# Kernel tuning notes

Hardware: AMD Instinct MI355X
Metric: run time of the kernel (lower is better)

The kernel has to match this reference:

```python
import jax, jax.numpy as jnp
import numpy as np

N_MESH, N_GRID, N_EDGE = 2562, 16384, 49152
D, EDGE_DIM, OUT_DIM = 512, 4, 128
LN_EPS = 1e-5


def _mlp_ln(x, w1, b1, w2, b2, g, beta):
    # Linear -> ReLU -> Linear -> LayerNorm (activate_final=False, use_layer_norm=True)
    h = jax.nn.relu(x @ w1 + b1)
    h = h @ w2 + b2
    mu = jnp.mean(h, axis=-1, keepdims=True)
    var = jnp.var(h, axis=-1, keepdims=True)
    return (h - mu) * jax.lax.rsqrt(var + LN_EPS) * g + beta


def setup_inputs() -> dict:
    key = jax.random.key(0)
    ks = iter(jax.random.split(key, 40))

    def W(i, o):
        return (jax.random.normal(next(ks), (i, o), jnp.float32) / np.float32(np.sqrt(i)))

    inp = {
        "input_mesh_nodes": jax.random.normal(next(ks), (N_MESH, D), jnp.float32),
        "input_grid_nodes": jax.random.normal(next(ks), (N_GRID, D), jnp.float32),
        "input_edge_attr": jax.random.normal(next(ks), (N_EDGE, EDGE_DIM), jnp.float32),
        "edge_index": jnp.stack([
            jax.random.randint(next(ks), (N_EDGE,), 0, N_MESH, jnp.int32),  # senders (mesh)
            jax.random.randint(next(ks), (N_EDGE,), 0, N_GRID, jnp.int32),  # receivers (grid)
        ], axis=0),
        # edges_mlp: EDGE_DIM -> D -> D, LN
        "emlp_w1": W(EDGE_DIM, D), "emlp_b1": jnp.zeros((D,), jnp.float32),
        "emlp_w2": W(D, D), "emlp_b2": jnp.zeros((D,), jnp.float32),
        "emlp_g": jnp.ones((D,), jnp.float32), "emlp_beta": jnp.zeros((D,), jnp.float32),
        # gnn message MLP: 3D -> D -> D, LN   (cat(x_i, x_j, edge_attr))
        "ge_w1": W(3 * D, D), "ge_b1": jnp.zeros((D,), jnp.float32),
        "ge_w2": W(D, D), "ge_b2": jnp.zeros((D,), jnp.float32),
        "ge_g": jnp.ones((D,), jnp.float32), "ge_beta": jnp.zeros((D,), jnp.float32),
        # gnn node MLP: 2D -> D -> D, LN   (cat(receiver_x, aggr))
        "gn_w1": W(2 * D, D), "gn_b1": jnp.zeros((D,), jnp.float32),
        "gn_w2": W(D, D), "gn_b2": jnp.zeros((D,), jnp.float32),
        "gn_g": jnp.ones((D,), jnp.float32), "gn_beta": jnp.zeros((D,), jnp.float32),
        # grid_mlp_final: D -> D -> OUT_DIM, LN
        "fin_w1": W(D, D), "fin_b1": jnp.zeros((D,), jnp.float32),
        "fin_w2": W(D, OUT_DIM), "fin_b2": jnp.zeros((OUT_DIM,), jnp.float32),
        "fin_g": jnp.ones((OUT_DIM,), jnp.float32), "fin_beta": jnp.zeros((OUT_DIM,), jnp.float32),
    }
    return inp


def reference(input_mesh_nodes, input_grid_nodes, input_edge_attr, edge_index,
              emlp_w1, emlp_b1, emlp_w2, emlp_b2, emlp_g, emlp_beta,
              ge_w1, ge_b1, ge_w2, ge_b2, ge_g, ge_beta,
              gn_w1, gn_b1, gn_w2, gn_b2, gn_g, gn_beta,
              fin_w1, fin_b1, fin_w2, fin_b2, fin_g, fin_beta):
    # edge embedding MLP
    edges_emb = _mlp_ln(input_edge_attr, emlp_w1, emlp_b1, emlp_w2, emlp_b2, emlp_g, emlp_beta)
    senders, receivers = edge_index[0], edge_index[1]
    x_i = input_grid_nodes[receivers]   # receiver (grid) features gathered per edge
    x_j = input_mesh_nodes[senders]     # sender (mesh) features gathered per edge
    # per-edge message MLP on cat(x_i, x_j, edge_attr)
    msg = _mlp_ln(jnp.concatenate([x_i, x_j, edges_emb], axis=-1),
                  ge_w1, ge_b1, ge_w2, ge_b2, ge_g, ge_beta)  # [E, D]
    # scatter-add messages to receiver grid nodes (aggr='add')
    aggr = jax.ops.segment_sum(msg, receivers, num_segments=N_GRID)  # [N_GRID, D]
    # node update MLP on cat(receiver_x, aggr)
    gnn_out = _mlp_ln(jnp.concatenate([input_grid_nodes, aggr], axis=-1),
                      gn_w1, gn_b1, gn_w2, gn_b2, gn_g, gn_beta)
    latent_grid_nodes = input_grid_nodes + gnn_out  # residual
    return _mlp_ln(latent_grid_nodes, fin_w1, fin_b1, fin_w2, fin_b2, fin_g, fin_beta)
```

## Files before the change

kernel.cpp:

```cpp
#include <hip/hip_runtime.h>
#include <hip/hip_bf16.h>
#include <stdint.h>

#define LN_EPS 1e-5f

typedef __hip_bfloat16 bf16;
typedef short short8 __attribute__((ext_vector_type(8)));
typedef float f32x4 __attribute__((ext_vector_type(4)));

static __device__ __forceinline__ float bf2f(short s) {
    unsigned int u = ((unsigned int)(unsigned short)s) << 16;
    return __uint_as_float(u);
}
static __device__ __forceinline__ short f2bf(float x) {
    __hip_bfloat16 h = __float2bfloat16(x);
    return *reinterpret_cast<short*>(&h);
}

static __device__ __forceinline__ void gload16(const void* g, void* l) {
    __builtin_amdgcn_global_load_lds((const __attribute__((address_space(1))) void*)g,
                                     (__attribute__((address_space(3))) void*)l, 16, 0, 0);
}

struct TDesc { const float* src; bf16* dst; int K; int N; int kOff; const float* scale; };
struct TDescs { TDesc d[9]; };

__global__ void transpose_all_kernel(TDescs descs) {
    TDesc t = descs.d[blockIdx.z];
    int kb = blockIdx.x * 32, nb = blockIdx.y * 32;
    if (kb >= t.K || nb >= t.N) return;
    __shared__ float tile[32][33];
    int tx = threadIdx.x & 31, ty = threadIdx.x >> 5;
    for (int i = ty; i < 32; i += 8) {
        int k = kb + i, n = nb + tx;
        float v = (k < t.K && n < t.N) ? t.src[(size_t)(t.kOff + k) * t.N + n] : 0.f;
        if (t.scale && k < t.K) v *= t.scale[k];
        tile[i][tx] = v;
    }
    __syncthreads();
    for (int i = ty; i < 32; i += 8) {
        int n = nb + i, k = kb + tx;
        if (n < t.N && k < t.K)
            t.dst[(size_t)n * t.K + k] = __float2bfloat16(tile[tx][i]);
    }
}

__global__ void uv_kernel(const float* __restrict__ W, const float* __restrict__ g,
                          const float* __restrict__ be, float* __restrict__ u,
                          float* __restrict__ v) {
    int n = blockIdx.x * 256 + threadIdx.x;
    if (n >= 512) return;
    float su = 0.f, sv = 0.f;
    for (int k = 0; k < 512; k++) {
        float w = W[(size_t)(1024 + k) * 512 + n];
        su += g[k] * w;
        sv += be[k] * w;
    }
    u[n] = su;
    v[n] = sv;
}

__global__ void cvt_bf16_kernel(const float* __restrict__ src, bf16* __restrict__ dst, int n) {
    int i = blockIdx.x * 256 + threadIdx.x;
    int idx = i * 4;
    if (idx >= n) return;
    float4 v = *(const float4*)(src + idx);
    dst[idx + 0] = __float2bfloat16(v.x);
    dst[idx + 1] = __float2bfloat16(v.y);
    dst[idx + 2] = __float2bfloat16(v.z);
    dst[idx + 3] = __float2bfloat16(v.w);
}

__global__ void edge_l1_kernel(const float* __restrict__ attr, const float* __restrict__ w1,
                               const float* __restrict__ b1, bf16* __restrict__ h1, int E) {
    int e = blockIdx.x * 4 + (threadIdx.x >> 6);
    if (e >= E) return;
    int lane = threadIdx.x & 63;
    int d0 = lane * 8;
    float4 a = *(const float4*)(attr + (size_t)e * 4);
    float av[4] = {a.x, a.y, a.z, a.w};
    float s[8];
    {
        float4 c0 = *(const float4*)(b1 + d0), c1 = *(const float4*)(b1 + d0 + 4);
        s[0]=c0.x; s[1]=c0.y; s[2]=c0.z; s[3]=c0.w; s[4]=c1.x; s[5]=c1.y; s[6]=c1.z; s[7]=c1.w;
    }
#pragma unroll
    for (int k = 0; k < 4; k++) {
        float4 w0 = *(const float4*)(w1 + k * 512 + d0);
        float4 w1v = *(const float4*)(w1 + k * 512 + d0 + 4);
        float wv[8] = {w0.x, w0.y, w0.z, w0.w, w1v.x, w1v.y, w1v.z, w1v.w};
#pragma unroll
        for (int j = 0; j < 8; j++) s[j] += av[k] * wv[j];
    }
    short8 o;
#pragma unroll
    for (int j = 0; j < 8; j++) o[j] = f2bf(fmaxf(s[j], 0.f));
    *(short8*)(h1 + (size_t)e * 512 + d0) = o;
}

template <int EPI>
__global__ __launch_bounds__(512, 1) void gemm8_kernel(
    const bf16* __restrict__ A, const bf16* __restrict__ BT,
    const float* __restrict__ bias, bf16* __restrict__ C, int M, int N, int K,
    const bf16* __restrict__ gridp, const bf16* __restrict__ meshp,
    const int* __restrict__ send, const int* __restrict__ recv,
    const float2* __restrict__ stats, const float* __restrict__ uvec,
    const float* __restrict__ vvec) {
    __shared__ short SMEM[2 * (256 + 128) * 64];
    const int t = threadIdx.x;
    const int lane = t & 63, w = t >> 6;
    const int wm = w >> 1, wn = w & 1;
    const int lr = lane & 15, lh = lane >> 4;

    int gx = gridDim.x;
    int nwg = gx * gridDim.y;
    int orig = blockIdx.y * gx + blockIdx.x;
    int q = nwg >> 3, r = nwg & 7;
    int xcd = orig & 7, loc = orig >> 3;
    int wg = (xcd < r ? xcd * (q + 1) : r * (q + 1) + (xcd - r) * q) + loc;
    int bx = wg % gx, by = wg / gx;
    const int row0 = by * 256;
    const int col0 = bx * 128;

    const int sr3 = lane >> 3;
    const int su = (lane & 7) ^ sr3;
    const int scol = su * 8;
    const bf16* gaP[4];
    const bf16* gbP[2];
#pragma unroll
    for (int c = 0; c < 4; c++) {
        int ra = row0 + c * 64 + w * 8 + sr3; if (ra >= M) ra = M - 1;
        gaP[c] = A + (size_t)ra * K + scol;
    }
#pragma unroll
    for (int c = 0; c < 2; c++) {
        int rb = col0 + c * 64 + w * 8 + sr3; if (rb >= N) rb = N - 1;
        gbP[c] = BT + (size_t)rb * K + scol;
    }

    auto STAGE_A = [&](int b, int k0) {
        short* la = SMEM + b * 24576;
#pragma unroll
        for (int c = 0; c < 4; c++)
            gload16(gaP[c] + k0, la + (c * 64 + w * 8) * 64);
    };
    auto STAGE_B = [&](int b, int k0) {
        short* lb = SMEM + b * 24576 + 16384;
#pragma unroll
        for (int c = 0; c < 2; c++)
            gload16(gbP[c] + k0, lb + (c * 64 + w * 8) * 64);
    };

    f32x4 acc[4][4];
#pragma unroll
    for (int i = 0; i < 4; i++)
#pragma unroll
        for (int j = 0; j < 4; j++) acc[i][j] = {0.f, 0.f, 0.f, 0.f};

    const int T = K >> 6;
    STAGE_A(0, 0);
    STAGE_B(0, 0);

    for (int tt = 0; tt < T; ++tt) {
        const int bc = tt & 1;
        const int kn = (tt + 1) << 6;
        if (tt + 1 < T) {
            STAGE_A(bc ^ 1, kn);
            asm volatile("s_waitcnt vmcnt(4)" ::: "memory");
        } else {
            asm volatile("s_waitcnt vmcnt(0)" ::: "memory");
        }
        __builtin_amdgcn_s_barrier();

        const short* Ac = SMEM + bc * 24576;
        const short* Bc = Ac + 16384;

        {
            short8 af[4], bfv[4];
#pragma unroll
            for (int mf = 0; mf < 4; mf++) {
                int rowa = wm * 64 + mf * 16 + lr;
                int ua = lh ^ (rowa & 7);
                af[mf] = *(const short8*)&Ac[rowa * 64 + ua * 8];
            }
#pragma unroll
            for (int nf = 0; nf < 4; nf++) {
                int rowb = wn * 64 + nf * 16 + lr;
                int ub = lh ^ (rowb & 7);
                bfv[nf] = *(const short8*)&Bc[rowb * 64 + ub * 8];
            }
            asm volatile("" ::: "memory");
            __builtin_amdgcn_s_barrier();
            __builtin_amdgcn_s_setprio(1);
#pragma unroll
            for (int mf = 0; mf < 4; mf++)
#pragma unroll
                for (int nf = 0; nf < 4; nf++)
                    acc[mf][nf] = __builtin_amdgcn_mfma_f32_16x16x32_bf16(
                        af[mf], bfv[nf], acc[mf][nf], 0, 0, 0);
            __builtin_amdgcn_s_setprio(0);
        }
        if (tt + 1 < T) STAGE_B(bc ^ 1, kn);
        {
            short8 af[4], bfv[4];
#pragma unroll
            for (int mf = 0; mf < 4; mf++) {
                int rowa = wm * 64 + mf * 16 + lr;
                int ua = (4 + lh) ^ (rowa & 7);
                af[mf] = *(const short8*)&Ac[rowa * 64 + ua * 8];
            }
#pragma unroll
            for (int nf = 0; nf < 4; nf++) {
                int rowb = wn * 64 + nf * 16 + lr;
                int ub = (4 + lh) ^ (rowb & 7);
                bfv[nf] = *(const short8*)&Bc[rowb * 64 + ub * 8];
            }
            asm volatile("" ::: "memory");
            __builtin_amdgcn_s_barrier();
            __builtin_amdgcn_s_setprio(1);
#pragma unroll
            for (int mf = 0; mf < 4; mf++)
#pragma unroll
                for (int nf = 0; nf < 4; nf++)
                    acc[mf][nf] = __builtin_amdgcn_mfma_f32_16x16x32_bf16(
                        af[mf], bfv[nf], acc[mf][nf], 0, 0, 0);
            __builtin_amdgcn_s_setprio(0);
        }
        asm volatile("" ::: "memory");
        __builtin_amdgcn_s_barrier();
    }

    short* Cw = SMEM + w * (32 * 66);
    const int rgrp = lane >> 3, u = lane & 7;
#pragma unroll
    for (int hp = 0; hp < 2; hp++) {
#pragma unroll
        for (int mf2 = 0; mf2 < 2; mf2++) {
            int mf = hp * 2 + mf2;
#pragma unroll
            for (int nf = 0; nf < 4; nf++)
#pragma unroll
                for (int r2 = 0; r2 < 4; r2++) {
                    int rl = mf2 * 16 + lh * 4 + r2;
                    Cw[rl * 66 + nf * 16 + lr] = f2bf(acc[mf][nf][r2]);
                }
        }
#pragma unroll
        for (int rr = 0; rr < 4; rr++) {
            int rl = rr * 8 + rgrp;
            int grow = row0 + wm * 64 + hp * 32 + rl;
            int gcol = col0 + wn * 64 + u * 8;
            short8 vv = *(const short8*)&Cw[rl * 66 + u * 8];
            float vf[8];
#pragma unroll
            for (int j = 0; j < 8; j++) vf[j] = bf2f(vv[j]);
            if (EPI == 4) {
                int e = grow < M ? grow : M - 1;
                float2 st = stats[e];
                float rs = st.y, mrs = st.x * st.y;
                float4 u0 = *(const float4*)(uvec + gcol), u1 = *(const float4*)(uvec + gcol + 4);
                float4 v0 = *(const float4*)(vvec + gcol), v1 = *(const float4*)(vvec + gcol + 4);
                float uu[8] = {u0.x, u0.y, u0.z, u0.w, u1.x, u1.y, u1.z, u1.w};
                float vvv[8] = {v0.x, v0.y, v0.z, v0.w, v1.x, v1.y, v1.z, v1.w};
#pragma unroll
                for (int j = 0; j < 8; j++) vf[j] = rs * vf[j] - mrs * uu[j] + vvv[j];
            }
            if (EPI >= 1) {
                float4 c0 = *(const float4*)(bias + gcol);
                float4 c1 = *(const float4*)(bias + gcol + 4);
                float bb[8] = {c0.x, c0.y, c0.z, c0.w, c1.x, c1.y, c1.z, c1.w};
#pragma unroll
                for (int j = 0; j < 8; j++) vf[j] += bb[j];
            }
            if (EPI == 4) {
                int e = grow < M ? grow : M - 1;
                int rn = recv[e], sn = send[e];
                short8 gp = *(const short8*)(gridp + (size_t)rn * 512 + gcol);
                short8 mp = *(const short8*)(meshp + (size_t)sn * 512 + gcol);
#pragma unroll
                for (int j = 0; j < 8; j++) vf[j] += bf2f(gp[j]) + bf2f(mp[j]);
            }
            if (EPI == 2 || EPI == 4) {
#pragma unroll
                for (int j = 0; j < 8; j++) vf[j] = fmaxf(vf[j], 0.f);
            }
            short8 o;
#pragma unroll
            for (int j = 0; j < 8; j++) o[j] = f2bf(vf[j]);
            if (grow < M && gcol < N)
                *(short8*)(C + (size_t)grow * N + gcol) = o;
        }
    }
}

template <int EPI>
__global__ __launch_bounds__(256, 2) void gemm_bt_kernel(
    const bf16* __restrict__ A, const bf16* __restrict__ BT,
    const float* __restrict__ bias, bf16* __restrict__ C, int M, int N, int K,
    const float* __restrict__ fg, const float* __restrict__ fb,
    float* __restrict__ OutF) {
    __shared__ short SMEM[2 * 2 * 128 * 64];
    const int t = threadIdx.x;
    const int lane = t & 63, w = t >> 6;
    const int wm = w >> 1, wn = w & 1;
    const int lr = lane & 15, lh = lane >> 4;

    int gx = gridDim.x;
    int nwg = gx * gridDim.y;
    int orig = blockIdx.y * gx + blockIdx.x;
    int q = nwg >> 3, r = nwg & 7;
    int xcd = orig & 7, loc = orig >> 3;
    int wg = (xcd < r ? xcd * (q + 1) : r * (q + 1) + (xcd - r) * q) + loc;
    int bx = wg % gx, by = wg / gx;
    const int row0 = by * 128;
    const int col0 = bx * 128;

    const int sr3 = lane >> 3;
    const int su = (lane & 7) ^ sr3;
    const int srow = w * 32 + sr3;
    const int scol = su * 8;
    const bf16* gaP[4];
    const bf16* gbP[4];
#pragma unroll
    for (int i = 0; i < 4; i++) {
        int ra = row0 + srow + i * 8; if (ra >= M) ra = M - 1;
        int rb = col0 + srow + i * 8; if (rb >= N) rb = N - 1;
        gaP[i] = A + (size_t)ra * K + scol;
        gbP[i] = BT + (size_t)rb * K + scol;
    }

    auto STAGE = [&](int b, int k0) {
        short* la = SMEM + b * 16384 + w * 32 * 64;
        short* lb = la + 8192;
#pragma unroll
        for (int i = 0; i < 4; i++) {
            gload16(gaP[i] + k0, la + i * 8 * 64);
            gload16(gbP[i] + k0, lb + i * 8 * 64);
        }
    };

    f32x4 acc[4][4];
#pragma unroll
    for (int i = 0; i < 4; i++)
#pragma unroll
        for (int j = 0; j < 4; j++) acc[i][j] = {0.f, 0.f, 0.f, 0.f};

    const int T = K >> 6;
    STAGE(0, 0);

    int cur = 0;
    for (int tt = 0; tt < T; ++tt) {
        if (tt + 1 < T) {
            STAGE(cur ^ 1, (tt + 1) << 6);
            asm volatile("s_waitcnt vmcnt(8)" ::: "memory");
        } else {
            asm volatile("s_waitcnt vmcnt(0)" ::: "memory");
        }
        __builtin_amdgcn_s_barrier();
        asm volatile("" ::: "memory");

        const short* Ac = SMEM + cur * 16384;
        const short* Bc = Ac + 8192;
#pragma unroll
        for (int kk = 0; kk < 64; kk += 32) {
            short8 af[4], bfv[4];
#pragma unroll
            for (int mf = 0; mf < 4; mf++) {
                int rowa = wm * 64 + mf * 16 + lr;
                int ua = ((kk >> 3) + lh) ^ (rowa & 7);
                af[mf] = *(const short8*)&Ac[rowa * 64 + ua * 8];
            }
#pragma unroll
            for (int nf = 0; nf < 4; nf++) {
                int rowb = wn * 64 + nf * 16 + lr;
                int ub = ((kk >> 3) + lh) ^ (rowb & 7);
                bfv[nf] = *(const short8*)&Bc[rowb * 64 + ub * 8];
            }
#pragma unroll
            for (int mf = 0; mf < 4; mf++)
#pragma unroll
                for (int nf = 0; nf < 4; nf++)
                    acc[mf][nf] = __builtin_amdgcn_mfma_f32_16x16x32_bf16(
                        af[mf], bfv[nf], acc[mf][nf], 0, 0, 0);
        }
        asm volatile("" ::: "memory");
        __builtin_amdgcn_s_barrier();
        cur ^= 1;
    }

    if (EPI == 5) {
        short* Cs = SMEM;
#pragma unroll
        for (int nf = 0; nf < 4; nf++) {
            float bv = bias[wn * 64 + nf * 16 + lr];
#pragma unroll
            for (int mf = 0; mf < 4; mf++)
#pragma unroll
                for (int r2 = 0; r2 < 4; r2++) {
                    int rl = wm * 64 + mf * 16 + lh * 4 + r2;
                    Cs[rl * 132 + wn * 64 + nf * 16 + lr] = f2bf(acc[mf][nf][r2] + bv);
                }
        }
        __syncthreads();
        int rl = w * 32 + (lane >> 1);
        int half = lane & 1;
        short8 vs[8];
        float s = 0.f, s2 = 0.f;
#pragma unroll
        for (int j8 = 0; j8 < 8; j8++) {
            vs[j8] = *(const short8*)&Cs[rl * 132 + half * 64 + j8 * 8];
#pragma unroll
            for (int j = 0; j < 8; j++) {
                float f = bf2f(vs[j8][j]);
                s += f; s2 += f * f;
            }
        }
        s += __shfl_xor(s, 1, 64);
        s2 += __shfl_xor(s2, 1, 64);
        float mu = s * (1.f / 128.f);
        float var = s2 * (1.f / 128.f) - mu * mu;
        float rs = rsqrtf(var + LN_EPS);
        int grow = row0 + rl;
#pragma unroll
        for (int j8 = 0; j8 < 8; j8++) {
            int c0 = half * 64 + j8 * 8;
            float4 g0 = *(const float4*)(fg + c0), g1 = *(const float4*)(fg + c0 + 4);
            float4 b0 = *(const float4*)(fb + c0), b1v = *(const float4*)(fb + c0 + 4);
            float gg[8] = {g0.x, g0.y, g0.z, g0.w, g1.x, g1.y, g1.z, g1.w};
            float bb[8] = {b0.x, b0.y, b0.z, b0.w, b1v.x, b1v.y, b1v.z, b1v.w};
            float4 o0, o1;
#pragma unroll
            for (int j = 0; j < 8; j++) {
                float y = (bf2f(vs[j8][j]) - mu) * rs * gg[j] + bb[j];
                if (j < 4) ((float*)&o0)[j] = y; else ((float*)&o1)[j - 4] = y;
            }
            *(float4*)(OutF + (size_t)grow * 128 + c0) = o0;
            *(float4*)(OutF + (size_t)grow * 128 + c0 + 4) = o1;
        }
        return;
    }

    short* Cw = SMEM + w * (32 * 66);
    const int rgrp = lane >> 3, u = lane & 7;
#pragma unroll
    for (int hp = 0; hp < 2; hp++) {
#pragma unroll
        for (int mf2 = 0; mf2 < 2; mf2++) {
            int mf = hp * 2 + mf2;
#pragma unroll
            for (int nf = 0; nf < 4; nf++)
#pragma unroll
                for (int r2 = 0; r2 < 4; r2++) {
                    int rl = mf2 * 16 + lh * 4 + r2;
                    Cw[rl * 66 + nf * 16 + lr] = f2bf(acc[mf][nf][r2]);
                }
        }
#pragma unroll
        for (int rr = 0; rr < 4; rr++) {
            int rl = rr * 8 + rgrp;
            int grow = row0 + wm * 64 + hp * 32 + rl;
            int gcol = col0 + wn * 64 + u * 8;
            short8 vv = *(const short8*)&Cw[rl * 66 + u * 8];
            if (grow < M && gcol < N)
                *(short8*)(C + (size_t)grow * N + gcol) = vv;
        }
    }
}

__global__ void ln_resid_kernel(const bf16* __restrict__ X, const float* __restrict__ gw,
                                const float* __restrict__ bw, bf16* __restrict__ outb,
                                const bf16* __restrict__ resid, int R) {
    int row = blockIdx.x * 4 + (threadIdx.x >> 6);
    if (row >= R) return;
    int lane = threadIdx.x & 63;
    short8 t8 = *(const short8*)(X + (size_t)row * 512 + lane * 8);
    float v[8];
#pragma unroll
    for (int j = 0; j < 8; j++) v[j] = bf2f(t8[j]);
    float s = 0.f, s2 = 0.f;
#pragma unroll
    for (int j = 0; j < 8; j++) { s += v[j]; s2 += v[j] * v[j]; }
#pragma unroll
    for (int o = 32; o > 0; o >>= 1) {
        s += __shfl_xor(s, o, 64);
        s2 += __shfl_xor(s2, o, 64);
    }
    float mu = s * (1.f / 512.f);
    float var = s2 * (1.f / 512.f) - mu * mu;
    float rs = rsqrtf(var + LN_EPS);
    int d0 = lane * 8;
    short8 rv = *(const short8*)(resid + (size_t)row * 512 + d0);
    short8 o;
#pragma unroll
    for (int j = 0; j < 8; j++) {
        float y = (v[j] - mu) * rs * gw[d0 + j] + bw[d0 + j];
        o[j] = f2bf(bf2f(rv[j]) + y);
    }
    *(short8*)(outb + (size_t)row * 512 + d0) = o;
}

__global__ void ln_stats_kernel(const bf16* __restrict__ X, float2* __restrict__ stats, int R) {
    int row = blockIdx.x * 4 + (threadIdx.x >> 6);
    if (row >= R) return;
    int lane = threadIdx.x & 63;
    short8 t8 = *(const short8*)(X + (size_t)row * 512 + lane * 8);
    float s = 0.f, s2 = 0.f;
#pragma unroll
    for (int j = 0; j < 8; j++) {
        float x = bf2f(t8[j]);
        s += x; s2 += x * x;
    }
#pragma unroll
    for (int o = 32; o > 0; o >>= 1) {
        s += __shfl_xor(s, o, 64);
        s2 += __shfl_xor(s2, o, 64);
    }
    float mu = s * (1.f / 512.f);
    float var = s2 * (1.f / 512.f) - mu * mu;
    if (lane == 0) stats[row] = make_float2(mu, rsqrtf(var + LN_EPS));
}

__global__ void degree_kernel(const int* __restrict__ recv, int* __restrict__ deg, int E) {
    int e = blockIdx.x * 256 + threadIdx.x;
    if (e < E) atomicAdd(&deg[recv[e]], 1);
}

__global__ void scan_kernel(const int* __restrict__ deg, int* __restrict__ off) {
    __shared__ int partial[1024];
    int t = threadIdx.x;
    int base = t * 16;
    int v[16];
    int s = 0;
#pragma unroll
    for (int i = 0; i < 16; i++) { v[i] = deg[base + i]; s += v[i]; }
    partial[t] = s;
    __syncthreads();
    for (int o = 1; o < 1024; o <<= 1) {
        int x = (t >= o) ? partial[t - o] : 0;
        __syncthreads();
        partial[t] += x;
        __syncthreads();
    }
    int run = (t == 0) ? 0 : partial[t - 1];
#pragma unroll
    for (int i = 0; i < 16; i++) { off[base + i] = run; run += v[i]; }
    if (t == 1023) off[16384] = run;
}

__global__ void scatter_kernel(const int* __restrict__ recv, const int* __restrict__ off,
                               int* __restrict__ cnt, int* __restrict__ edges, int E) {
    int e = blockIdx.x * 256 + threadIdx.x;
    if (e < E) {
        int r = recv[e];
        int p = atomicAdd(&cnt[r], 1);
        edges[off[r] + p] = e;
    }
}

__global__ void aggregate_kernel(const bf16* __restrict__ T5, const float2* __restrict__ stats,
                                 const float* __restrict__ gw, const float* __restrict__ bw,
                                 const bf16* __restrict__ gridb,
                                 const int* __restrict__ off, const int* __restrict__ edges,
                                 bf16* __restrict__ X2, int G) {
    int g = blockIdx.x * 4 + (threadIdx.x >> 6);
    if (g >= G) return;
    int lane = threadIdx.x & 63;
    int d0 = lane * 8;
    float gg[8], bb[8];
    {
        float4 a = *(const float4*)(gw + d0), b = *(const float4*)(gw + d0 + 4);
        gg[0]=a.x; gg[1]=a.y; gg[2]=a.z; gg[3]=a.w; gg[4]=b.x; gg[5]=b.y; gg[6]=b.z; gg[7]=b.w;
        float4 c = *(const float4*)(bw + d0), d = *(const float4*)(bw + d0 + 4);
        bb[0]=c.x; bb[1]=c.y; bb[2]=c.z; bb[3]=c.w; bb[4]=d.x; bb[5]=d.y; bb[6]=d.z; bb[7]=d.w;
    }
    float s[8] = {0.f, 0.f, 0.f, 0.f, 0.f, 0.f, 0.f, 0.f};
    int a = off[g], b = off[g + 1];
    for (int i = a; i < b; i++) {
        int e = edges[i];
        float2 st = stats[e];
        short8 m = *(const short8*)(T5 + (size_t)e * 512 + d0);
#pragma unroll
        for (int j = 0; j < 8; j++)
            s[j] += (bf2f(m[j]) - st.x) * st.y * gg[j] + bb[j];
    }
    *(short8*)(X2 + (size_t)g * 1024 + d0) = *(const short8*)(gridb + (size_t)g * 512 + d0);
    short8 o;
#pragma unroll
    for (int j = 0; j < 8; j++) o[j] = f2bf(s[j]);
    *(short8*)(X2 + (size_t)g * 1024 + 512 + d0) = o;
}

extern "C" void kernel_launch(void* const* d_in, const int* in_sizes, int n_in,
                              void* d_out, int out_size, void* d_ws, size_t ws_size,
                              hipStream_t stream) {
    const int NM = 2562, NG = 16384, NE = 49152;
    const float* mesh   = (const float*)d_in[0];
    const float* grid   = (const float*)d_in[1];
    const float* attr   = (const float*)d_in[2];
    const int*   eidx   = (const int*)d_in[3];
    const int*   send   = eidx;
    const int*   recv   = eidx + NE;
    const float* emlp_w1 = (const float*)d_in[4];
    const float* emlp_b1 = (const float*)d_in[5];
    const float* emlp_w2 = (const float*)d_in[6];
    const float* emlp_b2 = (const float*)d_in[7];
    const float* emlp_g  = (const float*)d_in[8];
    const float* emlp_be = (const float*)d_in[9];
    const float* ge_w1 = (const float*)d_in[10];
    const float* ge_b1 = (const float*)d_in[11];
    const float* ge_w2 = (const float*)d_in[12];
    const float* ge_b2 = (const float*)d_in[13];
    const float* ge_g  = (const float*)d_in[14];
    const float* ge_be = (const float*)d_in[15];
    const float* gn_w1 = (const float*)d_in[16];
    const float* gn_b1 = (const float*)d_in[17];
    const float* gn_w2 = (const float*)d_in[18];
    const float* gn_b2 = (const float*)d_in[19];
    const float* gn_g  = (const float*)d_in[20];
    const float* gn_be = (const float*)d_in[21];
    const float* fin_w1 = (const float*)d_in[22];
    const float* fin_b1 = (const float*)d_in[23];
    const float* fin_w2 = (const float*)d_in[24];
    const float* fin_b2 = (const float*)d_in[25];
    const float* fin_g  = (const float*)d_in[26];
    const float* fin_be = (const float*)d_in[27];

    char* p = (char*)d_ws;
    auto take = [&](size_t bytes) -> char* {
        char* r = p;
        p += (bytes + 255) & ~(size_t)255;
        return r;
    };
    bf16* emlp_w2T = (bf16*)take((size_t)512 * 512 * 2);
    bf16* geA_T    = (bf16*)take((size_t)512 * 512 * 2);
    bf16* geB_T    = (bf16*)take((size_t)512 * 512 * 2);
    bf16* geC_T    = (bf16*)take((size_t)512 * 512 * 2);
    bf16* ge_w2T   = (bf16*)take((size_t)512 * 512 * 2);
    bf16* gn_w1T   = (bf16*)take((size_t)512 * 1024 * 2);
    bf16* gn_w2T   = (bf16*)take((size_t)512 * 512 * 2);
    bf16* fin_w1T  = (bf16*)take((size_t)512 * 512 * 2);
    bf16* fin_w2T  = (bf16*)take((size_t)128 * 512 * 2);
    bf16* grid_bf  = (bf16*)take((size_t)NG * 512 * 2);
    bf16* mesh_bf  = (bf16*)take((size_t)NM * 512 * 2);
    bf16* bufA     = (bf16*)take((size_t)NE * 512 * 2);
    bf16* bufB     = (bf16*)take((size_t)NE * 512 * 2);
    bf16* bufC     = (bf16*)take((size_t)NG * 512 * 2);
    bf16* bufD     = (bf16*)take((size_t)NM * 512 * 2);
    float2* stats  = (float2*)take((size_t)NE * 8);
    float* uvecW   = (float*)take((size_t)512 * 4);
    float* vvecW   = (float*)take((size_t)512 * 4);
    int*  deg      = (int*)take((size_t)NG * 4);
    int*  cnt      = (int*)take((size_t)NG * 4);
    int*  csr_off  = (int*)take((size_t)(NG + 1) * 4);
    int*  csr_edge = (int*)take((size_t)NE * 4);

    const bf16* nbf = nullptr; const int* ni = nullptr;
    const float2* nst = nullptr; const float* nf = nullptr;

    TDescs td;
    td.d[0] = {emlp_w2, emlp_w2T, 512, 512, 0, nullptr};
    td.d[1] = {ge_w1,   geA_T,    512, 512, 0, nullptr};
    td.d[2] = {ge_w1,   geB_T,    512, 512, 512, nullptr};
    td.d[3] = {ge_w1,   geC_T,    512, 512, 1024, emlp_g};
    td.d[4] = {ge_w2,   ge_w2T,   512, 512, 0, nullptr};
    td.d[5] = {gn_w1,   gn_w1T,  1024, 512, 0, nullptr};
    td.d[6] = {gn_w2,   gn_w2T,   512, 512, 0, nullptr};
    td.d[7] = {fin_w1,  fin_w1T,  512, 512, 0, nullptr};
    td.d[8] = {fin_w2,  fin_w2T,  512, 128, 0, nullptr};
    hipLaunchKernelGGL(transpose_all_kernel, dim3(32, 16, 9), dim3(256), 0, stream, td);
    hipLaunchKernelGGL(uv_kernel, dim3(2), dim3(256), 0, stream,
                       ge_w1, emlp_g, emlp_be, uvecW, vvecW);

    hipLaunchKernelGGL(cvt_bf16_kernel, dim3((NG * 512 / 4 + 255) / 256), dim3(256), 0, stream,
                       grid, grid_bf, NG * 512);
    hipLaunchKernelGGL(cvt_bf16_kernel, dim3((NM * 512 / 4 + 255) / 256), dim3(256), 0, stream,
                       mesh, mesh_bf, NM * 512);
    hipMemsetAsync(deg, 0, (size_t)NG * 4, stream);
    hipMemsetAsync(cnt, 0, (size_t)NG * 4, stream);
    hipLaunchKernelGGL(degree_kernel, dim3((NE + 255) / 256), dim3(256), 0, stream, recv, deg, NE);
    hipLaunchKernelGGL(scan_kernel, dim3(1), dim3(1024), 0, stream, deg, csr_off);
    hipLaunchKernelGGL(scatter_kernel, dim3((NE + 255) / 256), dim3(256), 0, stream,
                       recv, csr_off, cnt, csr_edge, NE);

    hipLaunchKernelGGL(edge_l1_kernel, dim3(NE / 4), dim3(256), 0, stream,
                       attr, emlp_w1, emlp_b1, bufA, NE);
    hipLaunchKernelGGL(gemm8_kernel<1>, dim3(4, NE / 256), dim3(512), 0, stream,
                       bufA, emlp_w2T, emlp_b2, bufB, NE, 512, 512,
                       nbf, nbf, ni, ni, nst, nf, nf);
    hipLaunchKernelGGL(ln_stats_kernel, dim3(NE / 4), dim3(256), 0, stream, bufB, stats, NE);

    hipLaunchKernelGGL(gemm8_kernel<0>, dim3(4, NG / 256), dim3(512), 0, stream,
                       grid_bf, geA_T, nf, bufC, NG, 512, 512,
                       nbf, nbf, ni, ni, nst, nf, nf);
    hipLaunchKernelGGL(gemm_bt_kernel<0>, dim3(4, (NM + 127) / 128), dim3(256), 0, stream,
                       mesh_bf, geB_T, nf, bufD, NM, 512, 512, nf, nf, (float*)nullptr);
    hipLaunchKernelGGL(gemm8_kernel<4>, dim3(4, NE / 256), dim3(512), 0, stream,
                       bufB, geC_T, ge_b1, bufA, NE, 512, 512,
                       bufC, bufD, send, recv, stats, uvecW, vvecW);
    hipLaunchKernelGGL(gemm8_kernel<1>, dim3(4, NE / 256), dim3(512), 0, stream,
                       bufA, ge_w2T, ge_b2, bufB, NE, 512, 512,
                       nbf, nbf, ni, ni, nst, nf, nf);
    hipLaunchKernelGGL(ln_stats_kernel, dim3(NE / 4), dim3(256), 0, stream, bufB, stats, NE);
    hipLaunchKernelGGL(aggregate_kernel, dim3(NG / 4), dim3(256), 0, stream,
                       bufB, stats, ge_g, ge_be, grid_bf, csr_off, csr_edge, bufA, NG);

    hipLaunchKernelGGL(gemm8_kernel<2>, dim3(4, NG / 256), dim3(512), 0, stream,
                       bufA, gn_w1T, gn_b1, bufC, NG, 512, 1024,
                       nbf, nbf, ni, ni, nst, nf, nf);
    hipLaunchKernelGGL(gemm8_kernel<1>, dim3(4, NG / 256), dim3(512), 0, stream,
                       bufC, gn_w2T, gn_b2, bufB, NG, 512, 512,
                       nbf, nbf, ni, ni, nst, nf, nf);
    hipLaunchKernelGGL(ln_resid_kernel, dim3(NG / 4), dim3(256), 0, stream,
                       bufB, gn_g, gn_be, bufA, grid_bf, NG);

    hipLaunchKernelGGL(gemm8_kernel<2>, dim3(4, NG / 256), dim3(512), 0, stream,
                       bufA, fin_w1T, fin_b1, bufC, NG, 512, 512,
                       nbf, nbf, ni, ni, nst, nf, nf);
    hipLaunchKernelGGL(gemm_bt_kernel<5>, dim3(1, NG / 128), dim3(256), 0, stream,
                       bufC, fin_w2T, fin_b2, (bf16*)nullptr, NG, 128, 512,
                       fin_g, fin_be, (float*)d_out);
}
```

Measured before the change: 359.6 us.

## Single-buffer GEMM tiles for higher occupancy and route node GEMMs to 128-row kernel

After: 979.0 us. +172.2%, slower.

```diff
diff --git a/kernel.cpp b/kernel.cpp
--- a/kernel.cpp
+++ b/kernel.cpp
@@ -99,14 +99,14 @@
 }
 
 template <int EPI>
-__global__ __launch_bounds__(512, 1) void gemm8_kernel(
+__global__ __launch_bounds__(512, 6) void gemm256_kernel(
     const bf16* __restrict__ A, const bf16* __restrict__ BT,
     const float* __restrict__ bias, bf16* __restrict__ C, int M, int N, int K,
     const bf16* __restrict__ gridp, const bf16* __restrict__ meshp,
     const int* __restrict__ send, const int* __restrict__ recv,
     const float2* __restrict__ stats, const float* __restrict__ uvec,
     const float* __restrict__ vvec) {
-    __shared__ short SMEM[2 * (256 + 128) * 64];
+    __shared__ short SMEM[384 * 64];
     const int t = threadIdx.x;
     const int lane = t & 63, w = t >> 6;
     const int wm = w >> 1, wn = w & 1;
@@ -125,31 +125,18 @@
     const int sr3 = lane >> 3;
     const int su = (lane & 7) ^ sr3;
     const int scol = su * 8;
-    const bf16* gaP[4];
-    const bf16* gbP[2];
-#pragma unroll
-    for (int c = 0; c < 4; c++) {
-        int ra = row0 + c * 64 + w * 8 + sr3; if (ra >= M) ra = M - 1;
-        gaP[c] = A + (size_t)ra * K + scol;
-    }
-#pragma unroll
-    for (int c = 0; c < 2; c++) {
-        int rb = col0 + c * 64 + w * 8 + sr3; if (rb >= N) rb = N - 1;
-        gbP[c] = BT + (size_t)rb * K + scol;
-    }
-
-    auto STAGE_A = [&](int b, int k0) {
-        short* la = SMEM + b * 24576;
-#pragma unroll
-        for (int c = 0; c < 4; c++)
-            gload16(gaP[c] + k0, la + (c * 64 + w * 8) * 64);
-    };
-    auto STAGE_B = [&](int b, int k0) {
-        short* lb = SMEM + b * 24576 + 16384;
-#pragma unroll
-        for (int c = 0; c < 2; c++)
-            gload16(gbP[c] + k0, lb + (c * 64 + w * 8) * 64);
-    };
+    const bf16* gp6[6];
+#pragma unroll
+    for (int i = 0; i < 6; i++) {
+        int rr = w * 48 + i * 8 + sr3;
+        if (rr < 256) {
+            int ra = row0 + rr; if (ra >= M) ra = M - 1;
+            gp6[i] = A + (size_t)ra * K + scol;
+        } else {
+            int rb = col0 + (rr - 256); if (rb >= N) rb = N - 1;
+            gp6[i] = BT + (size_t)rb * K + scol;
+        }
+    }
 
     f32x4 acc[4][4];
 #pragma unroll
@@ -157,77 +144,34 @@
 #pragma unroll
         for (int j = 0; j < 4; j++) acc[i][j] = {0.f, 0.f, 0.f, 0.f};
 
-    const int T = K >> 6;
-    STAGE_A(0, 0);
-    STAGE_B(0, 0);
-
-    for (int tt = 0; tt < T; ++tt) {
-        const int bc = tt & 1;
-        const int kn = (tt + 1) << 6;
-        if (tt + 1 < T) {
-            STAGE_A(bc ^ 1, kn);
-            asm volatile("s_waitcnt vmcnt(4)" ::: "memory");
-        } else {
-            asm volatile("s_waitcnt vmcnt(0)" ::: "memory");
-        }
-        __builtin_amdgcn_s_barrier();
-
-        const short* Ac = SMEM + bc * 24576;
-        const short* Bc = Ac + 16384;
-
-        {
+    for (int k0 = 0; k0 < K; k0 += 64) {
+#pragma unroll
+        for (int i = 0; i < 6; i++)
+            gload16(gp6[i] + k0, SMEM + (w * 48 + i * 8) * 64);
+        __syncthreads();
+#pragma unroll
+        for (int kk = 0; kk < 64; kk += 32) {
             short8 af[4], bfv[4];
 #pragma unroll
             for (int mf = 0; mf < 4; mf++) {
                 int rowa = wm * 64 + mf * 16 + lr;
-                int ua = lh ^ (rowa & 7);
-                af[mf] = *(const short8*)&Ac[rowa * 64 + ua * 8];
+                int ua = ((kk >> 3) + lh) ^ (rowa & 7);
+                af[mf] = *(const short8*)&SMEM[rowa * 64 + ua * 8];
             }
 #pragma unroll
             for (int nf = 0; nf < 4; nf++) {
-                int rowb = wn * 64 + nf * 16 + lr;
-                int ub = lh ^ (rowb & 7);
-                bfv[nf] = *(const short8*)&Bc[rowb * 64 + ub * 8];
-            }
-            asm volatile("" ::: "memory");
-            __builtin_amdgcn_s_barrier();
-            __builtin_amdgcn_s_setprio(1);
+                int rowb = 256 + wn * 64 + nf * 16 + lr;
+                int ub = ((kk >> 3) + lh) ^ (rowb & 7);
+                bfv[nf] = *(const short8*)&SMEM[rowb * 64 + ub * 8];
+            }
 #pragma unroll
             for (int mf = 0; mf < 4; mf++)
 #pragma unroll
                 for (int nf = 0; nf < 4; nf++)
                     acc[mf][nf] = __builtin_amdgcn_mfma_f32_16x16x32_bf16(
                         af[mf], bfv[nf], acc[mf][nf], 0, 0, 0);
-            __builtin_amdgcn_s_setprio(0);
-        }
-        if (tt + 1 < T) STAGE_B(bc ^ 1, kn);
-        {
-            short8 af[4], bfv[4];
-#pragma unroll
-            for (int mf = 0; mf < 4; mf++) {
-                int rowa = wm * 64 + mf * 16 + lr;
-                int ua = (4 + lh) ^ (rowa & 7);
-                af[mf] = *(const short8*)&Ac[rowa * 64 + ua * 8];
-            }
-#pragma unroll
-            for (int nf = 0; nf < 4; nf++) {
-                int rowb = wn * 64 + nf * 16 + lr;
-                int ub = (4 + lh) ^ (rowb & 7);
-                bfv[nf] = *(const short8*)&Bc[rowb * 64 + ub * 8];
-            }
-            asm volatile("" ::: "memory");
-            __builtin_amdgcn_s_barrier();
-            __builtin_amdgcn_s_setprio(1);
-#pragma unroll
-            for (int mf = 0; mf < 4; mf++)
-#pragma unroll
-                for (int nf = 0; nf < 4; nf++)
-                    acc[mf][nf] = __builtin_amdgcn_mfma_f32_16x16x32_bf16(
-                        af[mf], bfv[nf], acc[mf][nf], 0, 0, 0);
-            __builtin_amdgcn_s_setprio(0);
-        }
-        asm volatile("" ::: "memory");
-        __builtin_amdgcn_s_barrier();
+        }
+        __syncthreads();
     }
 
     short* Cw = SMEM + w * (32 * 66);
@@ -294,12 +238,12 @@
 }
 
 template <int EPI>
-__global__ __launch_bounds__(256, 2) void gemm_bt_kernel(
+__global__ __launch_bounds__(256, 4) void gemm_bt_kernel(
     const bf16* __restrict__ A, const bf16* __restrict__ BT,
     const float* __restrict__ bias, bf16* __restrict__ C, int M, int N, int K,
     const float* __restrict__ fg, const float* __restrict__ fb,
     float* __restrict__ OutF) {
-    __shared__ short SMEM[2 * 2 * 128 * 64];
+    __shared__ short SMEM[132 * 128 + 64];
     const int t = threadIdx.x;
     const int lane = t & 63, w = t >> 6;
     const int wm = w >> 1, wn = w & 1;
@@ -329,38 +273,21 @@
         gbP[i] = BT + (size_t)rb * K + scol;
     }
 
-    auto STAGE = [&](int b, int k0) {
-        short* la = SMEM + b * 16384 + w * 32 * 64;
+    f32x4 acc[4][4];
+#pragma unroll
+    for (int i = 0; i < 4; i++)
+#pragma unroll
+        for (int j = 0; j < 4; j++) acc[i][j] = {0.f, 0.f, 0.f, 0.f};
+
+    for (int k0 = 0; k0 < K; k0 += 64) {
+        short* la = SMEM + w * 32 * 64;
         short* lb = la + 8192;
 #pragma unroll
         for (int i = 0; i < 4; i++) {
             gload16(gaP[i] + k0, la + i * 8 * 64);
             gload16(gbP[i] + k0, lb + i * 8 * 64);
         }
-    };
-
-    f32x4 acc[4][4];
-#pragma unroll
-    for (int i = 0; i < 4; i++)
-#pragma unroll
-        for (int j = 0; j < 4; j++) acc[i][j] = {0.f, 0.f, 0.f, 0.f};
-
-    const int T = K >> 6;
-    STAGE(0, 0);
-
-    int cur = 0;
-    for (int tt = 0; tt < T; ++tt) {
-        if (tt + 1 < T) {
-            STAGE(cur ^ 1, (tt + 1) << 6);
-            asm volatile("s_waitcnt vmcnt(8)" ::: "memory");
-        } else {
-            asm volatile("s_waitcnt vmcnt(0)" ::: "memory");
-        }
-        __builtin_amdgcn_s_barrier();
-        asm volatile("" ::: "memory");
-
-        const short* Ac = SMEM + cur * 16384;
-        const short* Bc = Ac + 8192;
+        __syncthreads();
 #pragma unroll
         for (int kk = 0; kk < 64; kk += 32) {
             short8 af[4], bfv[4];
@@ -368,13 +295,13 @@
             for (int mf = 0; mf < 4; mf++) {
                 int rowa = wm * 64 + mf * 16 + lr;
                 int ua = ((kk >> 3) + lh) ^ (rowa & 7);
-                af[mf] = *(const short8*)&Ac[rowa * 64 + ua * 8];
+                af[mf] = *(const short8*)&SMEM[rowa * 64 + ua * 8];
             }
 #pragma unroll
             for (int nf = 0; nf < 4; nf++) {
                 int rowb = wn * 64 + nf * 16 + lr;
                 int ub = ((kk >> 3) + lh) ^ (rowb & 7);
-                bfv[nf] = *(const short8*)&Bc[rowb * 64 + ub * 8];
+                bfv[nf] = *(const short8*)&SMEM[8192 + rowb * 64 + ub * 8];
             }
 #pragma unroll
             for (int mf = 0; mf < 4; mf++)
@@ -383,9 +310,7 @@
                     acc[mf][nf] = __builtin_amdgcn_mfma_f32_16x16x32_bf16(
                         af[mf], bfv[nf], acc[mf][nf], 0, 0, 0);
         }
-        asm volatile("" ::: "memory");
-        __builtin_amdgcn_s_barrier();
-        cur ^= 1;
+        __syncthreads();
     }
 
     if (EPI == 5) {
@@ -461,8 +386,25 @@
             int grow = row0 + wm * 64 + hp * 32 + rl;
             int gcol = col0 + wn * 64 + u * 8;
             short8 vv = *(const short8*)&Cw[rl * 66 + u * 8];
+            float vf[8];
+#pragma unroll
+            for (int j = 0; j < 8; j++) vf[j] = bf2f(vv[j]);
+            if (EPI >= 1) {
+                float4 c0 = *(const float4*)(bias + gcol);
+                float4 c1 = *(const float4*)(bias + gcol + 4);
+                float bb[8] = {c0.x, c0.y, c0.z, c0.w, c1.x, c1.y, c1.z, c1.w};
+#pragma unroll
+                for (int j = 0; j < 8; j++) vf[j] += bb[j];
+            }
+            if (EPI == 2) {
+#pragma unroll
+                for (int j = 0; j < 8; j++) vf[j] = fmaxf(vf[j], 0.f);
+            }
+            short8 o;
+#pragma unroll
+            for (int j = 0; j < 8; j++) o[j] = f2bf(vf[j]);
             if (grow < M && gcol < N)
-                *(short8*)(C + (size_t)grow * N + gcol) = vv;
+                *(short8*)(C + (size_t)grow * N + gcol) = o;
         }
     }
 }
@@ -684,38 +626,34 @@
 
     hipLaunchKernelGGL(edge_l1_kernel, dim3(NE / 4), dim3(256), 0, stream,
                        attr, emlp_w1, emlp_b1, bufA, NE);
-    hipLaunchKernelGGL(gemm8_kernel<1>, dim3(4, NE / 256), dim3(512), 0, stream,
+    hipLaunchKernelGGL(gemm256_kernel<1>, dim3(4, NE / 256), dim3(512), 0, stream,
                        bufA, emlp_w2T, emlp_b2, bufB, NE, 512, 512,
                        nbf, nbf, ni, ni, nst, nf, nf);
     hipLaunchKernelGGL(ln_stats_kernel, dim3(NE / 4), dim3(256), 0, stream, bufB, stats, NE);
 
-    hipLaunchKernelGGL(gemm8_kernel<0>, dim3(4, NG / 256), dim3(512), 0, stream,
-                       grid_bf, geA_T, nf, bufC, NG, 512, 512,
-                       nbf, nbf, ni, ni, nst, nf, nf);
+    hipLaunchKernelGGL(gemm_bt_kernel<0>, dim3(4, NG / 128), dim3(256), 0, stream,
+                       grid_bf, geA_T, nf, bufC, NG, 512, 512, nf, nf, (float*)nullptr);
     hipLaunchKernelGGL(gemm_bt_kernel<0>, dim3(4, (NM + 127) / 128), dim3(256), 0, stream,
                        mesh_bf, geB_T, nf, bufD, NM, 512, 512, nf, nf, (float*)nullptr);
-    hipLaunchKernelGGL(gemm8_kernel<4>, dim3(4, NE / 256), dim3(512), 0, stream,
+    hipLaunchKernelGGL(gemm256_kernel<4>, dim3(4, NE / 256), dim3(512), 0, stream,
                        bufB, geC_T, ge_b1, bufA, NE, 512, 512,
                        bufC, bufD, send, recv, stats, uvecW, vvecW);
-    hipLaunchKernelGGL(gemm8_kernel<1>, dim3(4, NE / 256), dim3(512), 0, stream,
+    hipLaunchKernelGGL(gemm256_kernel<1>, dim3(4, NE / 256), dim3(512), 0, stream,
                        bufA, ge_w2T, ge_b2, bufB, NE, 512, 512,
                        nbf, nbf, ni, ni, nst, nf, nf);
     hipLaunchKernelGGL(ln_stats_kernel, dim3(NE / 4), dim3(256), 0, stream, bufB, stats, NE);
     hipLaunchKernelGGL(aggregate_kernel, dim3(NG / 4), dim3(256), 0, stream,
                        bufB, stats, ge_g, ge_be, grid_bf, csr_off, csr_edge, bufA, NG);
 
-    hipLaunchKernelGGL(gemm8_kernel<2>, dim3(4, NG / 256), dim3(512), 0, stream,
-                       bufA, gn_w1T, gn_b1, bufC, NG, 512, 1024,
-                       nbf, nbf, ni, ni, nst, nf, nf);
-    hipLaunchKernelGGL(gemm8_kernel<1>, dim3(4, NG / 256), dim3(512), 0, stream,
-                       bufC, gn_w2T, gn_b2, bufB, NG, 512, 512,
-                       nbf, nbf, ni, ni, nst, nf, nf);
+    hipLaunchKernelGGL(gemm_bt_kernel<2>, dim3(4, NG / 128), dim3(256), 0, stream,
+                       bufA, gn_w1T, gn_b1, bufC, NG, 512, 1024, nf, nf, (float*)nullptr);
+    hipLaunchKernelGGL(gemm_bt_kernel<1>, dim3(4, NG / 128), dim3(256), 0, stream,
+                       bufC, gn_w2T, gn_b2, bufB, NG, 512, 512, nf, nf, (float*)nullptr);
     hipLaunchKernelGGL(ln_resid_kernel, dim3(NG / 4), dim3(256), 0, stream,
                        bufB, gn_g, gn_be, bufA, grid_bf, NG);
 
-    hipLaunchKernelGGL(gemm8_kernel<2>, dim3(4, NG / 256), dim3(512), 0, stream,
-                       bufA, fin_w1T, fin_b1, bufC, NG, 512, 512,
-                       nbf, nbf, ni, ni, nst, nf, nf);
+    hipLaunchKernelGGL(gemm_bt_kernel<2>, dim3(4, NG / 128), dim3(256), 0, stream,
+                       bufA, fin_w1T, fin_b1, bufC, NG, 512, 512, nf, nf, (float*)nullptr);
     hipLaunchKernelGGL(gemm_bt_kernel<5>, dim3(1, NG / 128), dim3(256), 0, stream,
                        bufC, fin_w2T, fin_b2, (bf16*)nullptr, NG, 128, 512,
                        fin_g, fin_be, (float*)d_out);
```
